# Kernel tuning notes

Measured on AMD Instinct MI355X. Metric: run time of the kernel, lower is better.

Reference implementation:

```python
import jax, jax.numpy as jnp
import numpy as np
from jax.scipy.linalg import expm

N_QUBITS = 10
DIM = 2 ** N_QUBITS        # 1024, statevector dimension
N_GATES = 24
FEAT_LEN = 1000            # padded with zeros up to DIM (pad_with=0.0)


def setup_inputs() -> dict:
    key = jax.random.key(0)
    kf, kt, kr, ki = jax.random.split(key, 4)
    feature = jax.random.normal(kf, (FEAT_LEN,), dtype=jnp.float32)
    # theta param: (len(gate_indices), 1) as in nn.param('theta', ..., (K, 1))
    theta = jax.random.normal(kt, (N_GATES, 1), dtype=jnp.float32)
    # fixed ansatz generators (Hermitian after symmetrization in reference)
    gens_re = jax.random.normal(kr, (N_GATES, DIM, DIM), dtype=jnp.float32)
    gens_im = jax.random.normal(ki, (N_GATES, DIM, DIM), dtype=jnp.float32)
    return {"feature": feature, "theta": theta, "gens_re": gens_re, "gens_im": gens_im}


def reference(feature, theta, gens_re, gens_im):
    D = gens_re.shape[-1]
    # Hermitian generators G_k = (M + M^H)/2
    M = gens_re.astype(jnp.complex64) + 1j * gens_im.astype(jnp.complex64)
    G = 0.5 * (M + jnp.conj(jnp.swapaxes(M, -1, -2)))  # [K, D, D]

    # AmplitudeEmbedding: pad feature with zeros to D, then L2-normalize
    psi = jnp.zeros((D,), dtype=jnp.complex64)
    psi = psi.at[: feature.shape[0]].set(feature.astype(jnp.complex64))
    psi = psi / jnp.linalg.norm(psi)

    # U_k = expm(-1j * theta_k * G_k), batched over gates
    coeff = (-1j) * theta[:, 0].astype(jnp.complex64)  # [K]
    U = jax.vmap(expm)(coeff[:, None, None] * G)       # [K, D, D]

    # sequential application of gates to the state
    def step(p, Uk):
        return Uk @ p, None

    psi, _ = jax.lax.scan(step, psi, U)

    # qml.probs over all wires
    probs = jnp.abs(psi) ** 2
    return probs
```

## Files before the change

kernel.cpp:

```cpp
#include <hip/hip_runtime.h>
#include <math.h>

#define DIM      1024
#define K_GATES  24
#define NMAX     512
#define QUAD_M   2048
#define BBOUND   66.0f
#define ROWS     16
#define NBLOCKS  64
#define NTHREADS 1024

__device__ __forceinline__ float2 cohLoad(const float2* p) {
    unsigned long long v = __hip_atomic_load((const unsigned long long*)p,
                                             __ATOMIC_RELAXED, __HIP_MEMORY_SCOPE_AGENT);
    union { unsigned long long u; float2 f; } c; c.u = v; return c.f;
}
__device__ __forceinline__ void cohStore(float2* p, float2 val) {
    union { unsigned long long u; float2 f; } c; c.f = val;
    __hip_atomic_store((unsigned long long*)p, c.u,
                       __ATOMIC_RELAXED, __HIP_MEMORY_SCOPE_AGENT);
}

__global__ __launch_bounds__(1024) void init_state(const float* __restrict__ f,
                                                   int nfeat, float2* __restrict__ xbuf,
                                                   unsigned int* __restrict__ bar) {
    __shared__ float red[16];
    __shared__ float invn_s;
    int t = threadIdx.x;
    float v = (t < nfeat) ? f[t] : 0.f;
    float s = v * v;
    #pragma unroll
    for (int o = 1; o < 64; o <<= 1) s += __shfl_xor(s, o);
    if ((t & 63) == 0) red[t >> 6] = s;
    __syncthreads();
    if (t == 0) {
        float tot = 0.f;
        for (int i = 0; i < 16; i++) tot += red[i];
        invn_s = 1.0f / sqrtf(tot);
        *bar = 0u;
    }
    __syncthreads();
    xbuf[t] = make_float2(v * invn_s, 0.f);
}

__global__ __launch_bounds__(256) void bessel_coef(const float* __restrict__ theta,
                                                   float2* __restrict__ coefs) {
    int n = blockIdx.x;
    int k = blockIdx.y;
    double tau = (double)theta[k] * (double)BBOUND;
    int t = threadIdx.x;
    double acc = 0.0;
    #pragma unroll
    for (int i = 0; i < QUAD_M / 256; i++) {
        int j = t + 256 * i;
        double phi = (2.0 * M_PI / (double)QUAD_M) * (double)j;
        acc += cos((double)n * phi - tau * sin(phi));
    }
    #pragma unroll
    for (int o = 1; o < 64; o <<= 1) acc += __shfl_xor(acc, o);
    __shared__ double red[4];
    if ((t & 63) == 0) red[t >> 6] = acc;
    __syncthreads();
    if (t == 0) {
        double J = (red[0] + red[1] + red[2] + red[3]) / (double)QUAD_M;
        double f = (n == 0) ? 1.0 : 2.0;
        float cr = 0.f, cim = 0.f;
        switch (n & 3) {
            case 0: cr  =  (float)(f * J); break;
            case 1: cim = -(float)(f * J); break;
            case 2: cr  = -(float)(f * J); break;
            case 3: cim =  (float)(f * J); break;
        }
        coefs[k * NMAX + n] = make_float2(cr, cim);
    }
}

__global__ __launch_bounds__(NMAX) void trunc_len(const float2* __restrict__ coefs,
                                                  int* __restrict__ nterm) {
    int k = blockIdx.x;
    int t = threadIdx.x;
    float2 c = coefs[k * NMAX + t];
    float mag = fabsf(c.x) + fabsf(c.y);
    int myn = (mag > 5e-7f) ? t : 0;
    #pragma unroll
    for (int o = 1; o < 64; o <<= 1) myn = max(myn, __shfl_xor(myn, o));
    __shared__ int red[8];
    if ((t & 63) == 0) red[t >> 6] = myn;
    __syncthreads();
    if (t == 0) {
        int m = 1;
        for (int i = 0; i < 8; i++) m = max(m, red[i]);
        nterm[k] = min(m, NMAX - 1);
    }
}

__global__ __launch_bounds__(NTHREADS) void evolve(const float* __restrict__ gre,
                                                   const float* __restrict__ gim,
                                                   float2* __restrict__ xbuf,
                                                   const float2* __restrict__ coefs,
                                                   const int* __restrict__ nterm,
                                                   unsigned int* __restrict__ bar,
                                                   float* __restrict__ out) {
    __shared__ float2 Gs[ROWS * DIM];
    __shared__ float2 xs[DIM];
    const int t = threadIdx.x, b = blockIdx.x;
    const int wave = t >> 6, lane = t & 63;
    const int r0 = b * ROWS;
    const int r = r0 + wave;
    const float hB = 0.5f / BBOUND;

    int cur = 0;
    int eps = 0;
    float2 acc = make_float2(0.f, 0.f);

    auto gbar = [&]() {
        eps++;
        __syncthreads();
        if (t == 0) {
            __hip_atomic_fetch_add(bar, 1u, __ATOMIC_RELAXED, __HIP_MEMORY_SCOPE_AGENT);
            unsigned tgt = (unsigned)eps * NBLOCKS;
            while (__hip_atomic_load(bar, __ATOMIC_RELAXED, __HIP_MEMORY_SCOPE_AGENT) < tgt)
                __builtin_amdgcn_s_sleep(4);
        }
        __syncthreads();
    };

    for (int k = 0; k < K_GATES; k++) {
        const float* R = gre + (size_t)k * DIM * DIM;
        const float* I = gim + (size_t)k * DIM * DIM;

        {
            const float4* Rc = (const float4*)(R + (size_t)t * DIM + r0);
            const float4* Ic = (const float4*)(I + (size_t)t * DIM + r0);
            float4 ra0 = Rc[0], ra1 = Rc[1], ra2 = Rc[2], ra3 = Rc[3];
            float4 ia0 = Ic[0], ia1 = Ic[1], ia2 = Ic[2], ia3 = Ic[3];
            Gs[ 0 * DIM + t] = make_float2(hB * ra0.x, -hB * ia0.x);
            Gs[ 1 * DIM + t] = make_float2(hB * ra0.y, -hB * ia0.y);
            Gs[ 2 * DIM + t] = make_float2(hB * ra0.z, -hB * ia0.z);
            Gs[ 3 * DIM + t] = make_float2(hB * ra0.w, -hB * ia0.w);
            Gs[ 4 * DIM + t] = make_float2(hB * ra1.x, -hB * ia1.x);
            Gs[ 5 * DIM + t] = make_float2(hB * ra1.y, -hB * ia1.y);
            Gs[ 6 * DIM + t] = make_float2(hB * ra1.z, -hB * ia1.z);
            Gs[ 7 * DIM + t] = make_float2(hB * ra1.w, -hB * ia1.w);
            Gs[ 8 * DIM + t] = make_float2(hB * ra2.x, -hB * ia2.x);
            Gs[ 9 * DIM + t] = make_float2(hB * ra2.y, -hB * ia2.y);
            Gs[10 * DIM + t] = make_float2(hB * ra2.z, -hB * ia2.z);
            Gs[11 * DIM + t] = make_float2(hB * ra2.w, -hB * ia2.w);
            Gs[12 * DIM + t] = make_float2(hB * ra3.x, -hB * ia3.x);
            Gs[13 * DIM + t] = make_float2(hB * ra3.y, -hB * ia3.y);
            Gs[14 * DIM + t] = make_float2(hB * ra3.z, -hB * ia3.z);
            Gs[15 * DIM + t] = make_float2(hB * ra3.w, -hB * ia3.w);
        }
        __syncthreads();
        {
            const float4* Rr = (const float4*)(R + (size_t)r * DIM);
            const float4* Ir = (const float4*)(I + (size_t)r * DIM);
            float4* G4 = (float4*)(Gs + (size_t)wave * DIM);
            #pragma unroll
            for (int m = 0; m < 4; m++) {
                int i4 = lane + 64 * m;
                float4 rv = Rr[i4], iv = Ir[i4];
                float4 g0 = G4[2 * i4], g1 = G4[2 * i4 + 1];
                g0.x += hB * rv.x; g0.y += hB * iv.x;
                g0.z += hB * rv.y; g0.w += hB * iv.y;
                g1.x += hB * rv.z; g1.y += hB * iv.z;
                g1.z += hB * rv.w; g1.w += hB * iv.w;
                G4[2 * i4] = g0; G4[2 * i4 + 1] = g1;
            }
        }
        __syncthreads();

        const int N = nterm[k];
        const float2* C = coefs + (size_t)k * NMAX;

        float2 t_prev, t_cur;
        bool first = true;

        for (int n = 1; n <= N; n++) {
            xs[t] = cohLoad(&xbuf[cur * DIM + t]);
            __syncthreads();

            float sre = 0.f, sim = 0.f;
            {
                const float4* x4 = (const float4*)xs;
                const float4* g4 = (const float4*)(Gs + (size_t)wave * DIM);
                #pragma unroll
                for (int m = 0; m < 8; m++) {
                    int idx = lane + 64 * m;
                    float4 xv = x4[idx];
                    float4 gv = g4[idx];
                    sre += gv.x * xv.x - gv.y * xv.y + gv.z * xv.z - gv.w * xv.w;
                    sim += gv.x * xv.y + gv.y * xv.x + gv.z * xv.w + gv.w * xv.z;
                }
                #pragma unroll
                for (int o = 1; o < 64; o <<= 1) {
                    sre += __shfl_xor(sre, o);
                    sim += __shfl_xor(sim, o);
                }
            }
            float2 w = make_float2(sre, sim);

            float2 t_next;
            if (first) {
                t_prev = xs[r];
                t_next = w;
                float2 c0 = C[0], c1 = C[1];
                acc.x = c0.x * t_prev.x - c0.y * t_prev.y + c1.x * w.x - c1.y * w.y;
                acc.y = c0.x * t_prev.y + c0.y * t_prev.x + c1.x * w.y + c1.y * w.x;
                first = false;
            } else {
                t_next = make_float2(2.f * w.x - t_prev.x, 2.f * w.y - t_prev.y);
                float2 cn = C[n];
                acc.x += cn.x * t_next.x - cn.y * t_next.y;
                acc.y += cn.x * t_next.y + cn.y * t_next.x;
                t_prev = t_cur;
            }
            t_cur = t_next;

            if (lane == 0) cohStore(&xbuf[(cur ^ 1) * DIM + r], t_next);
            cur ^= 1;
            gbar();
        }

        if (lane == 0) cohStore(&xbuf[(cur ^ 1) * DIM + r], acc);
        cur ^= 1;
        gbar();
    }

    if (lane == 0) out[r] = acc.x * acc.x + acc.y * acc.y;
}

extern "C" void kernel_launch(void* const* d_in, const int* in_sizes, int n_in,
                              void* d_out, int out_size, void* d_ws, size_t ws_size,
                              hipStream_t stream) {
    const float* feat  = (const float*)d_in[0];
    const float* theta = (const float*)d_in[1];
    const float* gre   = (const float*)d_in[2];
    const float* gim   = (const float*)d_in[3];

    char* base = (char*)d_ws;
    float2*       xbuf  = (float2*)base;
    float2*       coefs = (float2*)(base + 2 * DIM * sizeof(float2));
    int*          nterm = (int*)(base + 2 * DIM * sizeof(float2)
                                 + K_GATES * NMAX * sizeof(float2));
    unsigned int* bar   = (unsigned int*)(base + 2 * DIM * sizeof(float2)
                                          + K_GATES * NMAX * sizeof(float2)
                                          + K_GATES * sizeof(int));
    float* outp = (float*)d_out;

    init_state<<<1, 1024, 0, stream>>>(feat, in_sizes[0], xbuf, bar);
    bessel_coef<<<dim3(NMAX, K_GATES), 256, 0, stream>>>(theta, coefs);
    trunc_len<<<K_GATES, NMAX, 0, stream>>>(coefs, nterm);

    void* args[] = {(void*)&gre, (void*)&gim, (void*)&xbuf,
                    (void*)&coefs, (void*)&nterm, (void*)&bar, (void*)&outp};
    hipLaunchCooperativeKernel((void*)evolve, dim3(NBLOCKS), dim3(NTHREADS),
                               args, 0, stream);
}
```

Measured before the change: 6.501 ms.

## Replace grid barrier with canary-flagged ring slots and register-resident generator rows

Removes the global atomic-counter barrier after every Chebyshev step. Consumers now poll an 8-deep ring of state slots until no canary sentinel remains, and each producer resets an older slot to the canary after reading. Generator rows are held in registers (4 rows per wave, 32 blocks of 512 threads) so each step reads the state directly from global memory with no shared-memory staging. The aim is to cut barrier latency on the serial recurrence, at the cost of high register pressure, busy-wait polling traffic, and reliance on a NaN-pattern canary never appearing as real data.

```diff
diff --git a/kernel.cpp b/kernel.cpp
--- a/kernel.cpp
+++ b/kernel.cpp
@@ -6,24 +6,24 @@
 #define NMAX     512
 #define QUAD_M   2048
 #define BBOUND   66.0f
-#define ROWS     16
-#define NBLOCKS  64
-#define NTHREADS 1024
-
-__device__ __forceinline__ float2 cohLoad(const float2* p) {
-    unsigned long long v = __hip_atomic_load((const unsigned long long*)p,
-                                             __ATOMIC_RELAXED, __HIP_MEMORY_SCOPE_AGENT);
-    union { unsigned long long u; float2 f; } c; c.u = v; return c.f;
-}
-__device__ __forceinline__ void cohStore(float2* p, float2 val) {
-    union { unsigned long long u; float2 f; } c; c.f = val;
-    __hip_atomic_store((unsigned long long*)p, c.u,
-                       __ATOMIC_RELAXED, __HIP_MEMORY_SCOPE_AGENT);
+#define RPB      32
+#define NBLOCKS  32
+#define NTHREADS 512
+#define PSLOT    8
+#define CANARY   0x7FBADEAD7FBADEADull
+
+union F2U { unsigned long long u; float2 f; };
+
+__device__ __forceinline__ unsigned long long ld64coh(const unsigned long long* p) {
+    return __hip_atomic_load(p, __ATOMIC_RELAXED, __HIP_MEMORY_SCOPE_AGENT);
+}
+__device__ __forceinline__ void st64coh(unsigned long long* p, unsigned long long v) {
+    __hip_atomic_store(p, v, __ATOMIC_RELAXED, __HIP_MEMORY_SCOPE_AGENT);
 }
 
 __global__ __launch_bounds__(1024) void init_state(const float* __restrict__ f,
-                                                   int nfeat, float2* __restrict__ xbuf,
-                                                   unsigned int* __restrict__ bar) {
+                                                   int nfeat,
+                                                   unsigned long long* __restrict__ slots) {
     __shared__ float red[16];
     __shared__ float invn_s;
     int t = threadIdx.x;
@@ -37,10 +37,12 @@
         float tot = 0.f;
         for (int i = 0; i < 16; i++) tot += red[i];
         invn_s = 1.0f / sqrtf(tot);
-        *bar = 0u;
-    }
-    __syncthreads();
-    xbuf[t] = make_float2(v * invn_s, 0.f);
+    }
+    __syncthreads();
+    F2U c; c.f = make_float2(v * invn_s, 0.f);
+    slots[t] = c.u;
+    #pragma unroll
+    for (int p = 1; p < PSLOT; p++) slots[(size_t)p * DIM + t] = CANARY;
 }
 
 __global__ __launch_bounds__(256) void bessel_coef(const float* __restrict__ theta,
@@ -94,140 +96,167 @@
     }
 }
 
-__global__ __launch_bounds__(NTHREADS) void evolve(const float* __restrict__ gre,
-                                                   const float* __restrict__ gim,
-                                                   float2* __restrict__ xbuf,
-                                                   const float2* __restrict__ coefs,
-                                                   const int* __restrict__ nterm,
-                                                   unsigned int* __restrict__ bar,
-                                                   float* __restrict__ out) {
-    __shared__ float2 Gs[ROWS * DIM];
-    __shared__ float2 xs[DIM];
+__global__ __launch_bounds__(NTHREADS, 2) void evolve(
+        const float* __restrict__ gre, const float* __restrict__ gim,
+        unsigned long long* __restrict__ slots,
+        const float2* __restrict__ coefs, const int* __restrict__ nterm,
+        float* __restrict__ out) {
+    __shared__ float2 Gs[16 * DIM];
     const int t = threadIdx.x, b = blockIdx.x;
     const int wave = t >> 6, lane = t & 63;
-    const int r0 = b * ROWS;
-    const int r = r0 + wave;
+    const int q = lane & 3;
+    const int r0 = b * RPB;
+    const int myrow = r0 + 16 * (q >> 1) + 8 * (q & 1) + wave;
     const float hB = 0.5f / BBOUND;
 
-    int cur = 0;
-    int eps = 0;
-    float2 acc = make_float2(0.f, 0.f);
-
-    auto gbar = [&]() {
-        eps++;
-        __syncthreads();
-        if (t == 0) {
-            __hip_atomic_fetch_add(bar, 1u, __ATOMIC_RELAXED, __HIP_MEMORY_SCOPE_AGENT);
-            unsigned tgt = (unsigned)eps * NBLOCKS;
-            while (__hip_atomic_load(bar, __ATOMIC_RELAXED, __HIP_MEMORY_SCOPE_AGENT) < tgt)
-                __builtin_amdgcn_s_sleep(4);
-        }
-        __syncthreads();
-    };
-
-    for (int k = 0; k < K_GATES; k++) {
+    float2 g[4][16];
+    float2 psi, acc, t_m1, t_m2;
+    { F2U c; c.u = ld64coh(slots + myrow); psi = c.f; }
+    asm volatile("s_waitcnt vmcnt(0)" ::: "memory");
+    acc = t_m1 = t_m2 = make_float2(0.f, 0.f);
+
+    int rho = 1;
+    for (int k = 0; k < K_GATES; ++k) {
         const float* R = gre + (size_t)k * DIM * DIM;
         const float* I = gim + (size_t)k * DIM * DIM;
 
-        {
-            const float4* Rc = (const float4*)(R + (size_t)t * DIM + r0);
-            const float4* Ic = (const float4*)(I + (size_t)t * DIM + r0);
-            float4 ra0 = Rc[0], ra1 = Rc[1], ra2 = Rc[2], ra3 = Rc[3];
-            float4 ia0 = Ic[0], ia1 = Ic[1], ia2 = Ic[2], ia3 = Ic[3];
-            Gs[ 0 * DIM + t] = make_float2(hB * ra0.x, -hB * ia0.x);
-            Gs[ 1 * DIM + t] = make_float2(hB * ra0.y, -hB * ia0.y);
-            Gs[ 2 * DIM + t] = make_float2(hB * ra0.z, -hB * ia0.z);
-            Gs[ 3 * DIM + t] = make_float2(hB * ra0.w, -hB * ia0.w);
-            Gs[ 4 * DIM + t] = make_float2(hB * ra1.x, -hB * ia1.x);
-            Gs[ 5 * DIM + t] = make_float2(hB * ra1.y, -hB * ia1.y);
-            Gs[ 6 * DIM + t] = make_float2(hB * ra1.z, -hB * ia1.z);
-            Gs[ 7 * DIM + t] = make_float2(hB * ra1.w, -hB * ia1.w);
-            Gs[ 8 * DIM + t] = make_float2(hB * ra2.x, -hB * ia2.x);
-            Gs[ 9 * DIM + t] = make_float2(hB * ra2.y, -hB * ia2.y);
-            Gs[10 * DIM + t] = make_float2(hB * ra2.z, -hB * ia2.z);
-            Gs[11 * DIM + t] = make_float2(hB * ra2.w, -hB * ia2.w);
-            Gs[12 * DIM + t] = make_float2(hB * ra3.x, -hB * ia3.x);
-            Gs[13 * DIM + t] = make_float2(hB * ra3.y, -hB * ia3.y);
-            Gs[14 * DIM + t] = make_float2(hB * ra3.z, -hB * ia3.z);
-            Gs[15 * DIM + t] = make_float2(hB * ra3.w, -hB * ia3.w);
+        for (int h = 0; h < 2; ++h) {
+            const int c0 = r0 + 16 * h;
+            __syncthreads();
+            #pragma unroll
+            for (int rep = 0; rep < 2; ++rep) {
+                const int i = t + 512 * rep;
+                const float4* Rc = (const float4*)(R + (size_t)i * DIM + c0);
+                const float4* Ic = (const float4*)(I + (size_t)i * DIM + c0);
+                float4 ra0 = Rc[0], ra1 = Rc[1], ra2 = Rc[2], ra3 = Rc[3];
+                float4 ia0 = Ic[0], ia1 = Ic[1], ia2 = Ic[2], ia3 = Ic[3];
+                Gs[ 0 * DIM + i] = make_float2(hB * ra0.x, -hB * ia0.x);
+                Gs[ 1 * DIM + i] = make_float2(hB * ra0.y, -hB * ia0.y);
+                Gs[ 2 * DIM + i] = make_float2(hB * ra0.z, -hB * ia0.z);
+                Gs[ 3 * DIM + i] = make_float2(hB * ra0.w, -hB * ia0.w);
+                Gs[ 4 * DIM + i] = make_float2(hB * ra1.x, -hB * ia1.x);
+                Gs[ 5 * DIM + i] = make_float2(hB * ra1.y, -hB * ia1.y);
+                Gs[ 6 * DIM + i] = make_float2(hB * ra1.z, -hB * ia1.z);
+                Gs[ 7 * DIM + i] = make_float2(hB * ra1.w, -hB * ia1.w);
+                Gs[ 8 * DIM + i] = make_float2(hB * ra2.x, -hB * ia2.x);
+                Gs[ 9 * DIM + i] = make_float2(hB * ra2.y, -hB * ia2.y);
+                Gs[10 * DIM + i] = make_float2(hB * ra2.z, -hB * ia2.z);
+                Gs[11 * DIM + i] = make_float2(hB * ra2.w, -hB * ia2.w);
+                Gs[12 * DIM + i] = make_float2(hB * ra3.x, -hB * ia3.x);
+                Gs[13 * DIM + i] = make_float2(hB * ra3.y, -hB * ia3.y);
+                Gs[14 * DIM + i] = make_float2(hB * ra3.z, -hB * ia3.z);
+                Gs[15 * DIM + i] = make_float2(hB * ra3.w, -hB * ia3.w);
+            }
+            __syncthreads();
+            #pragma unroll
+            for (int s = 0; s < 2; ++s) {
+                const int lr = wave + 8 * s;
+                const int grow = r0 + 16 * h + lr;
+                const float4* Rr = (const float4*)(R + (size_t)grow * DIM);
+                const float4* Ir = (const float4*)(I + (size_t)grow * DIM);
+                float4* G4 = (float4*)(Gs + (size_t)lr * DIM);
+                #pragma unroll
+                for (int m = 0; m < 4; ++m) {
+                    int i4 = lane + 64 * m;
+                    float4 rv = Rr[i4], iv = Ir[i4];
+                    float4 g0 = G4[2 * i4], g1 = G4[2 * i4 + 1];
+                    g0.x += hB * rv.x; g0.y += hB * iv.x;
+                    g0.z += hB * rv.y; g0.w += hB * iv.y;
+                    g1.x += hB * rv.z; g1.y += hB * iv.z;
+                    g1.z += hB * rv.w; g1.w += hB * iv.w;
+                    G4[2 * i4] = g0; G4[2 * i4 + 1] = g1;
+                }
+            }
+            __syncthreads();
+            #pragma unroll
+            for (int p = 0; p < 2; ++p) {
+                const int lr = wave + 8 * p;
+                #pragma unroll
+                for (int m = 0; m < 16; ++m)
+                    g[2 * h + p][m] = Gs[lr * DIM + lane + 64 * m];
+            }
         }
-        __syncthreads();
-        {
-            const float4* Rr = (const float4*)(R + (size_t)r * DIM);
-            const float4* Ir = (const float4*)(I + (size_t)r * DIM);
-            float4* G4 = (float4*)(Gs + (size_t)wave * DIM);
-            #pragma unroll
-            for (int m = 0; m < 4; m++) {
-                int i4 = lane + 64 * m;
-                float4 rv = Rr[i4], iv = Ir[i4];
-                float4 g0 = G4[2 * i4], g1 = G4[2 * i4 + 1];
-                g0.x += hB * rv.x; g0.y += hB * iv.x;
-                g0.z += hB * rv.y; g0.w += hB * iv.y;
-                g1.x += hB * rv.z; g1.y += hB * iv.z;
-                g1.z += hB * rv.w; g1.w += hB * iv.w;
-                G4[2 * i4] = g0; G4[2 * i4 + 1] = g1;
-            }
-        }
-        __syncthreads();
 
         const int N = nterm[k];
         const float2* C = coefs + (size_t)k * NMAX;
 
-        float2 t_prev, t_cur;
-        bool first = true;
-
-        for (int n = 1; n <= N; n++) {
-            xs[t] = cohLoad(&xbuf[cur * DIM + t]);
-            __syncthreads();
-
-            float sre = 0.f, sim = 0.f;
-            {
-                const float4* x4 = (const float4*)xs;
-                const float4* g4 = (const float4*)(Gs + (size_t)wave * DIM);
-                #pragma unroll
-                for (int m = 0; m < 8; m++) {
-                    int idx = lane + 64 * m;
-                    float4 xv = x4[idx];
-                    float4 gv = g4[idx];
-                    sre += gv.x * xv.x - gv.y * xv.y + gv.z * xv.z - gv.w * xv.w;
-                    sim += gv.x * xv.y + gv.y * xv.x + gv.z * xv.w + gv.w * xv.z;
+        for (int n = 1; n <= N + 1; ++n, ++rho) {
+            unsigned long long* src = slots + (size_t)((rho - 1) & (PSLOT - 1)) * DIM;
+            unsigned long long* dst = slots + (size_t)(rho & (PSLOT - 1)) * DIM;
+            unsigned long long* ra  = slots + (size_t)((rho - 2) & (PSLOT - 1)) * DIM;
+
+            unsigned long long v[16];
+            #pragma unroll
+            for (int m = 0; m < 16; ++m) v[m] = ld64coh(src + lane + 64 * m);
+            unsigned pend = 0u;
+            #pragma unroll
+            for (int m = 0; m < 16; ++m) pend |= (v[m] == CANARY) ? (1u << m) : 0u;
+            while (pend) {
+                #pragma unroll
+                for (int m = 0; m < 16; ++m)
+                    if (pend & (1u << m)) v[m] = ld64coh(src + lane + 64 * m);
+                #pragma unroll
+                for (int m = 0; m < 16; ++m)
+                    if (v[m] != CANARY) pend &= ~(1u << m);
+            }
+            asm volatile("" ::: "memory");
+
+            if (lane < 4) st64coh(ra + myrow, CANARY);
+
+            float2 pub;
+            if (n <= N) {
+                float sre0 = 0.f, sim0 = 0.f, sre1 = 0.f, sim1 = 0.f;
+                float sre2 = 0.f, sim2 = 0.f, sre3 = 0.f, sim3 = 0.f;
+                #pragma unroll
+                for (int m = 0; m < 16; ++m) {
+                    F2U c; c.u = v[m];
+                    const float xr = c.f.x, xi = c.f.y;
+                    sre0 += g[0][m].x * xr - g[0][m].y * xi;
+                    sim0 += g[0][m].x * xi + g[0][m].y * xr;
+                    sre1 += g[1][m].x * xr - g[1][m].y * xi;
+                    sim1 += g[1][m].x * xi + g[1][m].y * xr;
+                    sre2 += g[2][m].x * xr - g[2][m].y * xi;
+                    sim2 += g[2][m].x * xi + g[2][m].y * xr;
+                    sre3 += g[3][m].x * xr - g[3][m].y * xi;
+                    sim3 += g[3][m].x * xi + g[3][m].y * xr;
                 }
                 #pragma unroll
                 for (int o = 1; o < 64; o <<= 1) {
-                    sre += __shfl_xor(sre, o);
-                    sim += __shfl_xor(sim, o);
-                }
-            }
-            float2 w = make_float2(sre, sim);
-
-            float2 t_next;
-            if (first) {
-                t_prev = xs[r];
-                t_next = w;
-                float2 c0 = C[0], c1 = C[1];
-                acc.x = c0.x * t_prev.x - c0.y * t_prev.y + c1.x * w.x - c1.y * w.y;
-                acc.y = c0.x * t_prev.y + c0.y * t_prev.x + c1.x * w.y + c1.y * w.x;
-                first = false;
+                    sre0 += __shfl_xor(sre0, o); sim0 += __shfl_xor(sim0, o);
+                    sre1 += __shfl_xor(sre1, o); sim1 += __shfl_xor(sim1, o);
+                    sre2 += __shfl_xor(sre2, o); sim2 += __shfl_xor(sim2, o);
+                    sre3 += __shfl_xor(sre3, o); sim3 += __shfl_xor(sim3, o);
+                }
+                const float wre = (q == 0) ? sre0 : (q == 1) ? sre1 : (q == 2) ? sre2 : sre3;
+                const float wim = (q == 0) ? sim0 : (q == 1) ? sim1 : (q == 2) ? sim2 : sim3;
+
+                float2 tn;
+                if (n == 1) {
+                    tn = make_float2(wre, wim);
+                    const float2 c0 = C[0], c1 = C[1];
+                    acc.x = c0.x * psi.x - c0.y * psi.y + c1.x * wre - c1.y * wim;
+                    acc.y = c0.x * psi.y + c0.y * psi.x + c1.x * wim + c1.y * wre;
+                    t_m2 = psi;
+                } else {
+                    tn = make_float2(2.f * wre - t_m2.x, 2.f * wim - t_m2.y);
+                    const float2 cn = C[n];
+                    acc.x += cn.x * tn.x - cn.y * tn.y;
+                    acc.y += cn.x * tn.y + cn.y * tn.x;
+                    t_m2 = t_m1;
+                }
+                t_m1 = tn;
+                pub = tn;
             } else {
-                t_next = make_float2(2.f * w.x - t_prev.x, 2.f * w.y - t_prev.y);
-                float2 cn = C[n];
-                acc.x += cn.x * t_next.x - cn.y * t_next.y;
-                acc.y += cn.x * t_next.y + cn.y * t_next.x;
-                t_prev = t_cur;
-            }
-            t_cur = t_next;
-
-            if (lane == 0) cohStore(&xbuf[(cur ^ 1) * DIM + r], t_next);
-            cur ^= 1;
-            gbar();
+                pub = acc;
+                psi = acc;
+            }
+
+            if (lane < 4) { F2U c; c.f = pub; st64coh(dst + myrow, c.u); }
+            asm volatile("s_waitcnt vmcnt(0)" ::: "memory");
         }
-
-        if (lane == 0) cohStore(&xbuf[(cur ^ 1) * DIM + r], acc);
-        cur ^= 1;
-        gbar();
-    }
-
-    if (lane == 0) out[r] = acc.x * acc.x + acc.y * acc.y;
+    }
+
+    if (lane < 4) out[myrow] = psi.x * psi.x + psi.y * psi.y;
 }
 
 extern "C" void kernel_launch(void* const* d_in, const int* in_sizes, int n_in,
@@ -239,21 +268,18 @@
     const float* gim   = (const float*)d_in[3];
 
     char* base = (char*)d_ws;
-    float2*       xbuf  = (float2*)base;
-    float2*       coefs = (float2*)(base + 2 * DIM * sizeof(float2));
-    int*          nterm = (int*)(base + 2 * DIM * sizeof(float2)
-                                 + K_GATES * NMAX * sizeof(float2));
-    unsigned int* bar   = (unsigned int*)(base + 2 * DIM * sizeof(float2)
-                                          + K_GATES * NMAX * sizeof(float2)
-                                          + K_GATES * sizeof(int));
+    unsigned long long* slots = (unsigned long long*)base;
+    float2* coefs = (float2*)(base + (size_t)PSLOT * DIM * sizeof(unsigned long long));
+    int*    nterm = (int*)(base + (size_t)PSLOT * DIM * sizeof(unsigned long long)
+                           + (size_t)K_GATES * NMAX * sizeof(float2));
     float* outp = (float*)d_out;
 
-    init_state<<<1, 1024, 0, stream>>>(feat, in_sizes[0], xbuf, bar);
+    init_state<<<1, 1024, 0, stream>>>(feat, in_sizes[0], slots);
     bessel_coef<<<dim3(NMAX, K_GATES), 256, 0, stream>>>(theta, coefs);
     trunc_len<<<K_GATES, NMAX, 0, stream>>>(coefs, nterm);
 
-    void* args[] = {(void*)&gre, (void*)&gim, (void*)&xbuf,
-                    (void*)&coefs, (void*)&nterm, (void*)&bar, (void*)&outp};
+    void* args[] = {(void*)&gre, (void*)&gim, (void*)&slots,
+                    (void*)&coefs, (void*)&nterm, (void*)&outp};
     hipLaunchCooperativeKernel((void*)evolve, dim3(NBLOCKS), dim3(NTHREADS),
                                args, 0, stream);
 }
```

Result: slower. 19.93 ms (+206.6%).

## Replace grid barrier with canary-flagged multi-slot dataflow synchronization

Applied to the files above, without the earlier changes.

Drops the atomic-counter grid barrier that ran after every Chebyshev step. Each step now publishes its row results into one of eight rotating global slots. Consumers spin on a per-element canary value until the data appears, and they reset an older slot to the canary for reuse. This removes the all-block rendezvous and its sleep polling, so blocks can run ahead as soon as their inputs exist, at the cost of per-element spin loads and the risk of a result that happens to equal the canary bit pattern.

```diff
diff --git a/kernel.cpp b/kernel.cpp
--- a/kernel.cpp
+++ b/kernel.cpp
@@ -9,21 +9,21 @@
 #define ROWS     16
 #define NBLOCKS  64
 #define NTHREADS 1024
-
-__device__ __forceinline__ float2 cohLoad(const float2* p) {
-    unsigned long long v = __hip_atomic_load((const unsigned long long*)p,
-                                             __ATOMIC_RELAXED, __HIP_MEMORY_SCOPE_AGENT);
-    union { unsigned long long u; float2 f; } c; c.u = v; return c.f;
-}
-__device__ __forceinline__ void cohStore(float2* p, float2 val) {
-    union { unsigned long long u; float2 f; } c; c.f = val;
-    __hip_atomic_store((unsigned long long*)p, c.u,
-                       __ATOMIC_RELAXED, __HIP_MEMORY_SCOPE_AGENT);
+#define PSLOT    8
+#define CANARY   0x7FBADEAD7FBADEADull
+
+union F2U { unsigned long long u; float2 f; };
+
+__device__ __forceinline__ unsigned long long ld64coh(const unsigned long long* p) {
+    return __hip_atomic_load(p, __ATOMIC_RELAXED, __HIP_MEMORY_SCOPE_AGENT);
+}
+__device__ __forceinline__ void st64coh(unsigned long long* p, unsigned long long v) {
+    __hip_atomic_store(p, v, __ATOMIC_RELAXED, __HIP_MEMORY_SCOPE_AGENT);
 }
 
 __global__ __launch_bounds__(1024) void init_state(const float* __restrict__ f,
-                                                   int nfeat, float2* __restrict__ xbuf,
-                                                   unsigned int* __restrict__ bar) {
+                                                   int nfeat,
+                                                   unsigned long long* __restrict__ slots) {
     __shared__ float red[16];
     __shared__ float invn_s;
     int t = threadIdx.x;
@@ -37,10 +37,12 @@
         float tot = 0.f;
         for (int i = 0; i < 16; i++) tot += red[i];
         invn_s = 1.0f / sqrtf(tot);
-        *bar = 0u;
-    }
-    __syncthreads();
-    xbuf[t] = make_float2(v * invn_s, 0.f);
+    }
+    __syncthreads();
+    F2U c; c.f = make_float2(v * invn_s, 0.f);
+    slots[t] = c.u;
+    #pragma unroll
+    for (int p = 1; p < PSLOT; p++) slots[(size_t)p * DIM + t] = CANARY;
 }
 
 __global__ __launch_bounds__(256) void bessel_coef(const float* __restrict__ theta,
@@ -94,36 +96,22 @@
     }
 }
 
-__global__ __launch_bounds__(NTHREADS) void evolve(const float* __restrict__ gre,
-                                                   const float* __restrict__ gim,
-                                                   float2* __restrict__ xbuf,
-                                                   const float2* __restrict__ coefs,
-                                                   const int* __restrict__ nterm,
-                                                   unsigned int* __restrict__ bar,
-                                                   float* __restrict__ out) {
+__global__ __launch_bounds__(NTHREADS) void evolve(
+        const float* __restrict__ gre, const float* __restrict__ gim,
+        unsigned long long* __restrict__ slots,
+        const float2* __restrict__ coefs, const int* __restrict__ nterm,
+        float* __restrict__ out) {
     __shared__ float2 Gs[ROWS * DIM];
-    __shared__ float2 xs[DIM];
+    __shared__ float2 xs[2 * DIM];
     const int t = threadIdx.x, b = blockIdx.x;
     const int wave = t >> 6, lane = t & 63;
     const int r0 = b * ROWS;
     const int r = r0 + wave;
     const float hB = 0.5f / BBOUND;
 
-    int cur = 0;
-    int eps = 0;
     float2 acc = make_float2(0.f, 0.f);
-
-    auto gbar = [&]() {
-        eps++;
-        __syncthreads();
-        if (t == 0) {
-            __hip_atomic_fetch_add(bar, 1u, __ATOMIC_RELAXED, __HIP_MEMORY_SCOPE_AGENT);
-            unsigned tgt = (unsigned)eps * NBLOCKS;
-            while (__hip_atomic_load(bar, __ATOMIC_RELAXED, __HIP_MEMORY_SCOPE_AGENT) < tgt)
-                __builtin_amdgcn_s_sleep(4);
-        }
-        __syncthreads();
-    };
+    float2 t_m1 = acc, t_m2 = acc;
+    int rho = 1;
 
     for (int k = 0; k < K_GATES; k++) {
         const float* R = gre + (size_t)k * DIM * DIM;
@@ -173,16 +161,23 @@
         const int N = nterm[k];
         const float2* C = coefs + (size_t)k * NMAX;
 
-        float2 t_prev, t_cur;
-        bool first = true;
-
-        for (int n = 1; n <= N; n++) {
-            xs[t] = cohLoad(&xbuf[cur * DIM + t]);
+        for (int n = 1; n <= N + 1; ++n, ++rho) {
+            unsigned long long* src = slots + (size_t)((rho - 1) & (PSLOT - 1)) * DIM;
+            unsigned long long* dst = slots + (size_t)(rho & (PSLOT - 1)) * DIM;
+            unsigned long long* ra  = slots + (size_t)((rho - 2) & (PSLOT - 1)) * DIM;
+            float2* xsb = xs + (size_t)(rho & 1) * DIM;
+
+            unsigned long long u = ld64coh(src + t);
+            while (u == CANARY) u = ld64coh(src + t);
+            { F2U c; c.u = u; xsb[t] = c.f; }
             __syncthreads();
 
-            float sre = 0.f, sim = 0.f;
-            {
-                const float4* x4 = (const float4*)xs;
+            if (t < ROWS) st64coh(ra + r0 + t, CANARY);
+
+            float2 pub;
+            if (n <= N) {
+                float sre = 0.f, sim = 0.f;
+                const float4* x4 = (const float4*)xsb;
                 const float4* g4 = (const float4*)(Gs + (size_t)wave * DIM);
                 #pragma unroll
                 for (int m = 0; m < 8; m++) {
@@ -197,34 +192,30 @@
                     sre += __shfl_xor(sre, o);
                     sim += __shfl_xor(sim, o);
                 }
+
+                float2 tn;
+                if (n == 1) {
+                    tn = make_float2(sre, sim);
+                    float2 p0 = xsb[r];
+                    const float2 c0 = C[0], c1 = C[1];
+                    acc.x = c0.x * p0.x - c0.y * p0.y + c1.x * tn.x - c1.y * tn.y;
+                    acc.y = c0.x * p0.y + c0.y * p0.x + c1.x * tn.y + c1.y * tn.x;
+                    t_m2 = p0;
+                } else {
+                    tn = make_float2(2.f * sre - t_m2.x, 2.f * sim - t_m2.y);
+                    const float2 cn = C[n];
+                    acc.x += cn.x * tn.x - cn.y * tn.y;
+                    acc.y += cn.x * tn.y + cn.y * tn.x;
+                    t_m2 = t_m1;
+                }
+                t_m1 = tn;
+                pub = tn;
+            } else {
+                pub = acc;
             }
-            float2 w = make_float2(sre, sim);
-
-            float2 t_next;
-            if (first) {
-                t_prev = xs[r];
-                t_next = w;
-                float2 c0 = C[0], c1 = C[1];
-                acc.x = c0.x * t_prev.x - c0.y * t_prev.y + c1.x * w.x - c1.y * w.y;
-                acc.y = c0.x * t_prev.y + c0.y * t_prev.x + c1.x * w.y + c1.y * w.x;
-                first = false;
-            } else {
-                t_next = make_float2(2.f * w.x - t_prev.x, 2.f * w.y - t_prev.y);
-                float2 cn = C[n];
-                acc.x += cn.x * t_next.x - cn.y * t_next.y;
-                acc.y += cn.x * t_next.y + cn.y * t_next.x;
-                t_prev = t_cur;
-            }
-            t_cur = t_next;
-
-            if (lane == 0) cohStore(&xbuf[(cur ^ 1) * DIM + r], t_next);
-            cur ^= 1;
-            gbar();
-        }
-
-        if (lane == 0) cohStore(&xbuf[(cur ^ 1) * DIM + r], acc);
-        cur ^= 1;
-        gbar();
+
+            if (lane == 0) { F2U c; c.f = pub; st64coh(dst + r, c.u); }
+        }
     }
 
     if (lane == 0) out[r] = acc.x * acc.x + acc.y * acc.y;
@@ -239,21 +230,18 @@
     const float* gim   = (const float*)d_in[3];
 
     char* base = (char*)d_ws;
-    float2*       xbuf  = (float2*)base;
-    float2*       coefs = (float2*)(base + 2 * DIM * sizeof(float2));
-    int*          nterm = (int*)(base + 2 * DIM * sizeof(float2)
-                                 + K_GATES * NMAX * sizeof(float2));
-    unsigned int* bar   = (unsigned int*)(base + 2 * DIM * sizeof(float2)
-                                          + K_GATES * NMAX * sizeof(float2)
-                                          + K_GATES * sizeof(int));
+    unsigned long long* slots = (unsigned long long*)base;
+    float2* coefs = (float2*)(base + (size_t)PSLOT * DIM * sizeof(unsigned long long));
+    int*    nterm = (int*)(base + (size_t)PSLOT * DIM * sizeof(unsigned long long)
+                           + (size_t)K_GATES * NMAX * sizeof(float2));
     float* outp = (float*)d_out;
 
-    init_state<<<1, 1024, 0, stream>>>(feat, in_sizes[0], xbuf, bar);
+    init_state<<<1, 1024, 0, stream>>>(feat, in_sizes[0], slots);
     bessel_coef<<<dim3(NMAX, K_GATES), 256, 0, stream>>>(theta, coefs);
     trunc_len<<<K_GATES, NMAX, 0, stream>>>(coefs, nterm);
 
-    void* args[] = {(void*)&gre, (void*)&gim, (void*)&xbuf,
-                    (void*)&coefs, (void*)&nterm, (void*)&bar, (void*)&outp};
+    void* args[] = {(void*)&gre, (void*)&gim, (void*)&slots,
+                    (void*)&coefs, (void*)&nterm, (void*)&outp};
     hipLaunchCooperativeKernel((void*)evolve, dim3(NBLOCKS), dim3(NTHREADS),
                                args, 0, stream);
 }
```

Measured after the change: 8.074 ms. 1.24x slower.
